# Kernel tuning notes

Measured on AMD Instinct MI355X. Metric: run time of the kernel, lower is better.

Reference implementation:

```python
import jax, jax.numpy as jnp
import numpy as np

D = 1024
S = 4096

def setup_inputs() -> dict:
    key = jax.random.key(0)
    ks = jax.random.split(key, 7)
    x = jax.random.normal(ks[0], (S, D), dtype=jnp.float32)
    scale = 1.0 / np.sqrt(D)
    wq = jax.random.normal(ks[1], (D, D), dtype=jnp.float32) * scale
    wk = jax.random.normal(ks[2], (D, D), dtype=jnp.float32) * scale
    wv = jax.random.normal(ks[3], (D, D), dtype=jnp.float32) * scale
    bq = jax.random.normal(ks[4], (D,), dtype=jnp.float32) * 0.01
    bk = jax.random.normal(ks[5], (D,), dtype=jnp.float32) * 0.01
    bv = jax.random.normal(ks[6], (D,), dtype=jnp.float32) * 0.01
    return {"x": x, "wq": wq, "bq": bq, "wk": wk, "bk": bk, "wv": wv, "bv": bv}

def reference(x, wq, bq, wk, bk, wv, bv):
    # q = x @ wq^T + bq  (torch nn.Linear convention: weight [out,in])
    q = x @ wq.T + bq            # [S, D]
    k = x @ wk.T + bk            # [S, D]
    v = x @ wv.T + bv            # [S, D]
    inv_sqrt_d = 1.0 / jnp.sqrt(jnp.asarray(x.shape[1], dtype=x.dtype))
    scores = (q @ k.T) * inv_sqrt_d      # [S, S]
    attn = jax.nn.softmax(scores, axis=-1)
    return attn @ v                      # [S, D]
```

## Files before the change

kernel.cpp:

```cpp
#include <hip/hip_runtime.h>
#include <stdint.h>
#include <stddef.h>

#define SEQ 4096
#define DIM 1024

typedef __bf16 bf16x8 __attribute__((ext_vector_type(8)));
typedef float floatx4 __attribute__((ext_vector_type(4)));
typedef unsigned short u16x8 __attribute__((ext_vector_type(8)));

__device__ __forceinline__ unsigned short f2b(float f) {
  union { float f; unsigned u; } v; v.f = f;
  unsigned u = v.u;
  unsigned r = (u + 0x7FFFu + ((u >> 16) & 1u)) >> 16;
  return (unsigned short)r;
}
__device__ __forceinline__ float b2f(unsigned short h) {
  union { unsigned u; float f; } v; v.u = ((unsigned)h) << 16;
  return v.f;
}

__global__ __launch_bounds__(256)
void cvt_all(const float* __restrict__ x, const float* __restrict__ wq,
             const float* __restrict__ wk, const float* __restrict__ wv,
             unsigned short* __restrict__ xb, unsigned short* __restrict__ wqb,
             unsigned short* __restrict__ wkb, unsigned short* __restrict__ wvb) {
  const int bid = blockIdx.x;
  const float* src;
  unsigned short* dst;
  int off;
  if (bid < 4096)      { src = x;  dst = xb;  off = bid; }
  else if (bid < 5120) { src = wq; dst = wqb; off = bid - 4096; }
  else if (bid < 6144) { src = wk; dst = wkb; off = bid - 5120; }
  else                 { src = wv; dst = wvb; off = bid - 6144; }
  const int i = off * 1024 + threadIdx.x * 4;
  float4 f = *(const float4*)(src + i);
  ushort4 o;
  o.x = f2b(f.x); o.y = f2b(f.y); o.z = f2b(f.z); o.w = f2b(f.w);
  *(ushort4*)(dst + i) = o;
}

__device__ __forceinline__ void swizzle_tiles(int gx, int gy, int& bx, int& by) {
  const int pid = blockIdx.y * gx + blockIdx.x;
  const int GM = 8;
  const int group = pid / (GM * gx);
  const int first = group * GM;
  const int gsz = (gy - first) < GM ? (gy - first) : GM;
  by = first + (pid % gsz);
  bx = (pid % (GM * gx)) / gsz;
}

__device__ __forceinline__ void gemm_core128(
    const unsigned short* __restrict__ A,
    const unsigned short* __restrict__ B,
    int lda, int ldb, int kext,
    unsigned short* As, unsigned short* Bs,
    floatx4 acc[4][4]) {
  const int tid  = threadIdx.x;
  const int lane = tid & 63;
  const int wave = tid >> 6;
  const int sub_m = (wave >> 1) * 64;
  const int sub_n = (wave & 1) * 64;
  const int col  = lane & 15;
  const int quad = lane >> 4;

  const int srow  = tid >> 3;
  const int sgran = (tid & 7) ^ (srow & 7);
  const int scol  = sgran * 8;
  const int dflat = tid * 8;

  const unsigned short* Ag = A + (size_t)srow * lda + scol;
  const unsigned short* Bg = B + (size_t)srow * ldb + scol;

  for (int k0 = 0; k0 < kext; k0 += 64) {
    __syncthreads();
#pragma unroll
    for (int j = 0; j < 4; j++) {
      __builtin_amdgcn_global_load_lds(
          (const __attribute__((address_space(1))) void*)(Ag + (size_t)(j * 32) * lda + k0),
          (__attribute__((address_space(3))) void*)(&As[j * 2048 + dflat]), 16, 0, 0);
      __builtin_amdgcn_global_load_lds(
          (const __attribute__((address_space(1))) void*)(Bg + (size_t)(j * 32) * ldb + k0),
          (__attribute__((address_space(3))) void*)(&Bs[j * 2048 + dflat]), 16, 0, 0);
    }
    __syncthreads();
#pragma unroll
    for (int ks = 0; ks < 64; ks += 32) {
      const int gbase = ks >> 3;
      bf16x8 af[4], bfr[4];
#pragma unroll
      for (int i = 0; i < 4; i++) {
        const int R = sub_m + 16 * i + col;
        const int slot = (gbase + quad) ^ (R & 7);
        af[i] = *(const bf16x8*)&As[R * 64 + slot * 8];
      }
#pragma unroll
      for (int j = 0; j < 4; j++) {
        const int R = sub_n + 16 * j + col;
        const int slot = (gbase + quad) ^ (R & 7);
        bfr[j] = *(const bf16x8*)&Bs[R * 64 + slot * 8];
      }
#pragma unroll
      for (int i = 0; i < 4; i++)
#pragma unroll
        for (int j = 0; j < 4; j++)
          acc[i][j] = __builtin_amdgcn_mfma_f32_16x16x32_bf16(af[i], bfr[j],
                                                              acc[i][j], 0, 0, 0);
    }
  }
}


__global__ __launch_bounds__(256, 2)
void qkv_gemm(const unsigned short* __restrict__ xb,
              const unsigned short* __restrict__ wqb,
              const unsigned short* __restrict__ wkb,
              const unsigned short* __restrict__ wvb,
              const float* __restrict__ bq, const float* __restrict__ bk,
              const float* __restrict__ bv,
              unsigned short* __restrict__ qb, unsigned short* __restrict__ kb,
              unsigned short* __restrict__ vtb) {
  __shared__ unsigned short As[8192];
  __shared__ unsigned short Bs[8192];
  const int z = blockIdx.z;
  const int pid = blockIdx.x;

  floatx4 acc[4][4];
#pragma unroll
  for (int i = 0; i < 4; i++)
#pragma unroll
    for (int j = 0; j < 4; j++) acc[i][j] = (floatx4)0.0f;

  const int lane = threadIdx.x & 63;
  const int wave = threadIdx.x >> 6;
  const int sub_m = (wave >> 1) * 64;
  const int sub_n = (wave & 1) * 64;
  const int col  = lane & 15;
  const int quad = lane >> 4;

  if (z < 2) {
    const unsigned short* W = z ? wkb : wqb;
    const float* bias = z ? bk : bq;
    unsigned short* outp = z ? kb : qb;
    const int by = pid >> 3, bx = pid & 7;
    const int tile_m = by * 128, tile_n = bx * 128;

    gemm_core128(xb + (size_t)tile_m * DIM, W + (size_t)tile_n * DIM,
                 DIM, DIM, DIM, As, Bs, acc);

    float biasv[4];
#pragma unroll
    for (int j = 0; j < 4; j++) biasv[j] = bias[tile_n + sub_n + 16 * j + col];
#pragma unroll
    for (int i = 0; i < 4; i++)
#pragma unroll
      for (int j = 0; j < 4; j++)
#pragma unroll
        for (int r = 0; r < 4; r++) {
          const int m = tile_m + sub_m + 16 * i + quad * 4 + r;
          const int n = tile_n + sub_n + 16 * j + col;
          outp[(size_t)m * DIM + n] = f2b(acc[i][j][r] + biasv[j]);
        }
  } else {
    const int by = pid >> 5, bx = pid & 31;
    const int tile_m = by * 128, tile_n = bx * 128;

    gemm_core128(wvb + (size_t)tile_m * DIM, xb + (size_t)tile_n * DIM,
                 DIM, DIM, DIM, As, Bs, acc);

#pragma unroll
    for (int i = 0; i < 4; i++) {
      const float* bp = &bv[tile_m + sub_m + 16 * i + quad * 4];
      float bm[4];
#pragma unroll
      for (int r = 0; r < 4; r++) bm[r] = bp[r];
#pragma unroll
      for (int j = 0; j < 4; j++)
#pragma unroll
        for (int r = 0; r < 4; r++) {
          const int m = tile_m + sub_m + 16 * i + quad * 4 + r;
          const int n = tile_n + sub_n + 16 * j + col;
          vtb[(size_t)m * SEQ + n] = f2b(acc[i][j][r] + bm[r]);
        }
    }
  }
}

__global__ __launch_bounds__(256, 2)
void score_gemm(const unsigned short* __restrict__ qb,
                const unsigned short* __restrict__ kb,
                unsigned short* __restrict__ sc, float scale) {
  __shared__ unsigned short As[8192];
  __shared__ unsigned short Bs[8192];
  const int pid = blockIdx.y * gridDim.x + blockIdx.x;
  const int xcd = pid & 7;
  const int local = pid >> 3;
  const int bx = xcd * 4 + (local & 3);
  const int by = local >> 2;
  const int tile_m = by * 128;
  const int tile_n = bx * 128;

  floatx4 acc[4][4];
#pragma unroll
  for (int i = 0; i < 4; i++)
#pragma unroll
    for (int j = 0; j < 4; j++) acc[i][j] = (floatx4)0.0f;

  gemm_core128(qb + (size_t)tile_m * DIM, kb + (size_t)tile_n * DIM,
               DIM, DIM, DIM, As, Bs, acc);

  const int lane = threadIdx.x & 63;
  const int wave = threadIdx.x >> 6;
  const int sub_m = (wave >> 1) * 64;
  const int sub_n = (wave & 1) * 64;
  const int col  = lane & 15;
  const int quad = lane >> 4;
#pragma unroll
  for (int i = 0; i < 4; i++)
#pragma unroll
    for (int j = 0; j < 4; j++)
#pragma unroll
      for (int r = 0; r < 4; r++) {
        const int m = tile_m + sub_m + 16 * i + quad * 4 + r;
        const int n = tile_n + sub_n + 16 * j + col;
        sc[(size_t)m * SEQ + n] = f2b(acc[i][j][r] * scale);
      }
}

__global__ __launch_bounds__(256, 2)
void pv_gemm(const unsigned short* __restrict__ sc,
             const unsigned short* __restrict__ vtb,
             float* __restrict__ out0, float* __restrict__ out1) {
  __shared__ unsigned short As[8192];
  __shared__ unsigned short Bs[8192];
  const int z = blockIdx.z;
  const int koff = z * (SEQ / 2);
  float* C = z ? out1 : out0;
  int bx, by;
  swizzle_tiles(gridDim.x, gridDim.y, bx, by);
  const int tile_m = by * 128;
  const int tile_n = bx * 128;

  floatx4 acc[4][4];
#pragma unroll
  for (int i = 0; i < 4; i++)
#pragma unroll
    for (int j = 0; j < 4; j++) acc[i][j] = (floatx4)0.0f;

  gemm_core128(sc + (size_t)tile_m * SEQ + koff,
               vtb + (size_t)tile_n * SEQ + koff,
               SEQ, SEQ, SEQ / 2, As, Bs, acc);

  const int lane = threadIdx.x & 63;
  const int wave = threadIdx.x >> 6;
  const int sub_m = (wave >> 1) * 64;
  const int sub_n = (wave & 1) * 64;
  const int col  = lane & 15;
  const int quad = lane >> 4;
#pragma unroll
  for (int i = 0; i < 4; i++)
#pragma unroll
    for (int j = 0; j < 4; j++)
#pragma unroll
      for (int r = 0; r < 4; r++) {
        const int m = tile_m + sub_m + 16 * i + quad * 4 + r;
        const int n = tile_n + sub_n + 16 * j + col;
        C[(size_t)m * DIM + n] = acc[i][j][r];
      }
}

__global__ __launch_bounds__(256)
void reduce_add(float* __restrict__ out, const float* __restrict__ part) {
  const int i = (blockIdx.x * 256 + threadIdx.x) * 4;
  float4 a = *(const float4*)(out + i);
  float4 b = *(const float4*)(part + i);
  a.x += b.x; a.y += b.y; a.z += b.z; a.w += b.w;
  *(float4*)(out + i) = a;
}

__global__ __launch_bounds__(256)
void softmax_inplace(unsigned short* __restrict__ P) {
  const int row = blockIdx.x;
  unsigned short* p = P + (size_t)row * SEQ;
  const int tid  = threadIdx.x;
  const int lane = tid & 63;
  const int wave = tid >> 6;

  u16x8 raw0 = *(const u16x8*)(p + tid * 16);
  u16x8 raw1 = *(const u16x8*)(p + tid * 16 + 8);
  float v[16];
#pragma unroll
  for (int k = 0; k < 8; k++) v[k] = b2f(raw0[k]);
#pragma unroll
  for (int k = 0; k < 8; k++) v[8 + k] = b2f(raw1[k]);

  float mx = -1e30f;
#pragma unroll
  for (int k = 0; k < 16; k++) mx = fmaxf(mx, v[k]);
#pragma unroll
  for (int off = 32; off > 0; off >>= 1) mx = fmaxf(mx, __shfl_xor(mx, off, 64));
  __shared__ float redm[4];
  __shared__ float reds[4];
  if (lane == 0) redm[wave] = mx;
  __syncthreads();
  mx = fmaxf(fmaxf(redm[0], redm[1]), fmaxf(redm[2], redm[3]));

  float sum = 0.0f;
#pragma unroll
  for (int k = 0; k < 16; k++) {
    v[k] = exp2f((v[k] - mx) * 1.44269504f);
    sum += v[k];
  }
#pragma unroll
  for (int off = 32; off > 0; off >>= 1) sum += __shfl_xor(sum, off, 64);
  if (lane == 0) reds[wave] = sum;
  __syncthreads();
  sum = reds[0] + reds[1] + reds[2] + reds[3];
  const float inv = 1.0f / sum;

  u16x8 o0, o1;
#pragma unroll
  for (int k = 0; k < 8; k++) o0[k] = f2b(v[k] * inv);
#pragma unroll
  for (int k = 0; k < 8; k++) o1[k] = f2b(v[8 + k] * inv);
  *(u16x8*)(p + tid * 16) = o0;
  *(u16x8*)(p + tid * 16 + 8) = o1;
}

extern "C" void kernel_launch(void* const* d_in, const int* in_sizes, int n_in,
                              void* d_out, int out_size, void* d_ws, size_t ws_size,
                              hipStream_t stream) {
  const float* x  = (const float*)d_in[0];
  const float* wq = (const float*)d_in[1];
  const float* bq = (const float*)d_in[2];
  const float* wk = (const float*)d_in[3];
  const float* bk = (const float*)d_in[4];
  const float* wv = (const float*)d_in[5];
  const float* bv = (const float*)d_in[6];

  uint8_t* ws = (uint8_t*)d_ws;
  unsigned short* xb  = (unsigned short*)(ws);
  unsigned short* wqb = (unsigned short*)(ws + ((size_t)8  << 20));
  unsigned short* wkb = (unsigned short*)(ws + ((size_t)10 << 20));
  unsigned short* wvb = (unsigned short*)(ws + ((size_t)12 << 20));
  unsigned short* qb  = (unsigned short*)(ws + ((size_t)14 << 20));
  unsigned short* kb  = (unsigned short*)(ws + ((size_t)22 << 20));
  unsigned short* vtb = (unsigned short*)(ws + ((size_t)30 << 20));
  unsigned short* sc  = (unsigned short*)(ws + ((size_t)38 << 20));
  float*          part = (float*)(ws);

  cvt_all<<<7168, 256, 0, stream>>>(x, wq, wk, wv, xb, wqb, wkb, wvb);

  qkv_gemm<<<dim3(256, 1, 3), 256, 0, stream>>>(
      xb, wqb, wkb, wvb, bq, bk, bv, qb, kb, vtb);

  score_gemm<<<dim3(SEQ / 128, SEQ / 128), 256, 0, stream>>>(qb, kb, sc, 0.03125f);

  softmax_inplace<<<SEQ, 256, 0, stream>>>(sc);

  pv_gemm<<<dim3(DIM / 128, SEQ / 128, 2), 256, 0, stream>>>(
      sc, vtb, (float*)d_out, part);

  reduce_add<<<(SEQ * DIM) / 1024, 256, 0, stream>>>((float*)d_out, part);
}
```

Baseline: 205.6 us.

## Fuse softmax exp into score GEMM and normalize in PV epilogue with atomics

The score GEMM epilogue now applies exp2 to the scaled scores and accumulates per-row sums into a global buffer with atomics. The separate softmax kernel is removed, and the PV GEMM divides by the row sum in its epilogue. Its two K-split halves are combined with atomicAdd into a zeroed output instead of a reduce kernel. This drops a full read and write pass over the 4096x4096 score matrix and one launch. In exchange it skips max subtraction, which risks overflow for large scores, and adds global atomics on the row sums and the output.

```diff
diff --git a/kernel.cpp b/kernel.cpp
--- a/kernel.cpp
+++ b/kernel.cpp
@@ -7,17 +7,12 @@
 
 typedef __bf16 bf16x8 __attribute__((ext_vector_type(8)));
 typedef float floatx4 __attribute__((ext_vector_type(4)));
-typedef unsigned short u16x8 __attribute__((ext_vector_type(8)));
 
 __device__ __forceinline__ unsigned short f2b(float f) {
   union { float f; unsigned u; } v; v.f = f;
   unsigned u = v.u;
   unsigned r = (u + 0x7FFFu + ((u >> 16) & 1u)) >> 16;
   return (unsigned short)r;
-}
-__device__ __forceinline__ float b2f(unsigned short h) {
-  union { unsigned u; float f; } v; v.u = ((unsigned)h) << 16;
-  return v.f;
 }
 
 __global__ __launch_bounds__(256)
@@ -189,7 +184,8 @@
 __global__ __launch_bounds__(256, 2)
 void score_gemm(const unsigned short* __restrict__ qb,
                 const unsigned short* __restrict__ kb,
-                unsigned short* __restrict__ sc, float scale) {
+                unsigned short* __restrict__ sc,
+                float* __restrict__ rsum, float c ) {
   __shared__ unsigned short As[8192];
   __shared__ unsigned short Bs[8192];
   const int pid = blockIdx.y * gridDim.x + blockIdx.x;
@@ -215,6 +211,31 @@
   const int sub_n = (wave & 1) * 64;
   const int col  = lane & 15;
   const int quad = lane >> 4;
+
+#pragma unroll
+  for (int i = 0; i < 4; i++)
+#pragma unroll
+    for (int j = 0; j < 4; j++)
+#pragma unroll
+      for (int r = 0; r < 4; r++)
+        acc[i][j][r] = exp2f(acc[i][j][r] * c);
+
+#pragma unroll
+  for (int i = 0; i < 4; i++) {
+#pragma unroll
+    for (int r = 0; r < 4; r++) {
+      float s = acc[i][0][r] + acc[i][1][r] + acc[i][2][r] + acc[i][3][r];
+      s += __shfl_xor(s, 1, 16);
+      s += __shfl_xor(s, 2, 16);
+      s += __shfl_xor(s, 4, 16);
+      s += __shfl_xor(s, 8, 16);
+      if (col == 0) {
+        const int m = tile_m + sub_m + 16 * i + quad * 4 + r;
+        atomicAdd(&rsum[m], s);
+      }
+    }
+  }
+
 #pragma unroll
   for (int i = 0; i < 4; i++)
 #pragma unroll
@@ -223,19 +244,19 @@
       for (int r = 0; r < 4; r++) {
         const int m = tile_m + sub_m + 16 * i + quad * 4 + r;
         const int n = tile_n + sub_n + 16 * j + col;
-        sc[(size_t)m * SEQ + n] = f2b(acc[i][j][r] * scale);
+        sc[(size_t)m * SEQ + n] = f2b(acc[i][j][r]);
       }
 }
 
 __global__ __launch_bounds__(256, 2)
 void pv_gemm(const unsigned short* __restrict__ sc,
              const unsigned short* __restrict__ vtb,
-             float* __restrict__ out0, float* __restrict__ out1) {
+             const float* __restrict__ rsum,
+             float* __restrict__ out) {
   __shared__ unsigned short As[8192];
   __shared__ unsigned short Bs[8192];
   const int z = blockIdx.z;
   const int koff = z * (SEQ / 2);
-  float* C = z ? out1 : out0;
   int bx, by;
   swizzle_tiles(gridDim.x, gridDim.y, bx, by);
   const int tile_m = by * 128;
@@ -257,6 +278,14 @@
   const int sub_n = (wave & 1) * 64;
   const int col  = lane & 15;
   const int quad = lane >> 4;
+
+  float invr[4][4];
+#pragma unroll
+  for (int i = 0; i < 4; i++)
+#pragma unroll
+    for (int r = 0; r < 4; r++)
+      invr[i][r] = 1.0f / rsum[tile_m + sub_m + 16 * i + quad * 4 + r];
+
 #pragma unroll
   for (int i = 0; i < 4; i++)
 #pragma unroll
@@ -265,66 +294,8 @@
       for (int r = 0; r < 4; r++) {
         const int m = tile_m + sub_m + 16 * i + quad * 4 + r;
         const int n = tile_n + sub_n + 16 * j + col;
-        C[(size_t)m * DIM + n] = acc[i][j][r];
-      }
-}
-
-__global__ __launch_bounds__(256)
-void reduce_add(float* __restrict__ out, const float* __restrict__ part) {
-  const int i = (blockIdx.x * 256 + threadIdx.x) * 4;
-  float4 a = *(const float4*)(out + i);
-  float4 b = *(const float4*)(part + i);
-  a.x += b.x; a.y += b.y; a.z += b.z; a.w += b.w;
-  *(float4*)(out + i) = a;
-}
-
-__global__ __launch_bounds__(256)
-void softmax_inplace(unsigned short* __restrict__ P) {
-  const int row = blockIdx.x;
-  unsigned short* p = P + (size_t)row * SEQ;
-  const int tid  = threadIdx.x;
-  const int lane = tid & 63;
-  const int wave = tid >> 6;
-
-  u16x8 raw0 = *(const u16x8*)(p + tid * 16);
-  u16x8 raw1 = *(const u16x8*)(p + tid * 16 + 8);
-  float v[16];
-#pragma unroll
-  for (int k = 0; k < 8; k++) v[k] = b2f(raw0[k]);
-#pragma unroll
-  for (int k = 0; k < 8; k++) v[8 + k] = b2f(raw1[k]);
-
-  float mx = -1e30f;
-#pragma unroll
-  for (int k = 0; k < 16; k++) mx = fmaxf(mx, v[k]);
-#pragma unroll
-  for (int off = 32; off > 0; off >>= 1) mx = fmaxf(mx, __shfl_xor(mx, off, 64));
-  __shared__ float redm[4];
-  __shared__ float reds[4];
-  if (lane == 0) redm[wave] = mx;
-  __syncthreads();
-  mx = fmaxf(fmaxf(redm[0], redm[1]), fmaxf(redm[2], redm[3]));
-
-  float sum = 0.0f;
-#pragma unroll
-  for (int k = 0; k < 16; k++) {
-    v[k] = exp2f((v[k] - mx) * 1.44269504f);
-    sum += v[k];
-  }
-#pragma unroll
-  for (int off = 32; off > 0; off >>= 1) sum += __shfl_xor(sum, off, 64);
-  if (lane == 0) reds[wave] = sum;
-  __syncthreads();
-  sum = reds[0] + reds[1] + reds[2] + reds[3];
-  const float inv = 1.0f / sum;
-
-  u16x8 o0, o1;
-#pragma unroll
-  for (int k = 0; k < 8; k++) o0[k] = f2b(v[k] * inv);
-#pragma unroll
-  for (int k = 0; k < 8; k++) o1[k] = f2b(v[8 + k] * inv);
-  *(u16x8*)(p + tid * 16) = o0;
-  *(u16x8*)(p + tid * 16 + 8) = o1;
+        atomicAdd(&out[(size_t)m * DIM + n], acc[i][j][r] * invr[i][r]);
+      }
 }
 
 extern "C" void kernel_launch(void* const* d_in, const int* in_sizes, int n_in,
@@ -347,19 +318,19 @@
   unsigned short* kb  = (unsigned short*)(ws + ((size_t)22 << 20));
   unsigned short* vtb = (unsigned short*)(ws + ((size_t)30 << 20));
   unsigned short* sc  = (unsigned short*)(ws + ((size_t)38 << 20));
-  float*          part = (float*)(ws);
+  float*          rsum = (float*)(ws + ((size_t)70 << 20));
+
+  hipMemsetAsync(rsum, 0, SEQ * sizeof(float), stream);
+  hipMemsetAsync(d_out, 0, (size_t)SEQ * DIM * sizeof(float), stream);
 
   cvt_all<<<7168, 256, 0, stream>>>(x, wq, wk, wv, xb, wqb, wkb, wvb);
 
   qkv_gemm<<<dim3(256, 1, 3), 256, 0, stream>>>(
       xb, wqb, wkb, wvb, bq, bk, bv, qb, kb, vtb);
 
-  score_gemm<<<dim3(SEQ / 128, SEQ / 128), 256, 0, stream>>>(qb, kb, sc, 0.03125f);
-
-  softmax_inplace<<<SEQ, 256, 0, stream>>>(sc);
+  score_gemm<<<dim3(SEQ / 128, SEQ / 128), 256, 0, stream>>>(
+      qb, kb, sc, rsum, 0.03125f * 1.44269504088896f);
 
   pv_gemm<<<dim3(DIM / 128, SEQ / 128, 2), 256, 0, stream>>>(
-      sc, vtb, (float*)d_out, part);
-
-  reduce_add<<<(SEQ * DIM) / 1024, 256, 0, stream>>>((float*)d_out, part);
-}
+      sc, vtb, rsum, (float*)d_out);
+}
```

Result: slower. 228.5 us (+11.1%).
